# Optimization experiments

Measured on AMD Instinct MI355X. Metric: run time of the kernel, lower is better.

Reference implementation:

```python
import jax, jax.numpy as jnp
import numpy as np
import math

H, D, DFF = 12, 768, 3072
DH = D // H  # 64
B, T = 4, 2048
EPS = 1e-5


def setup_inputs() -> dict:
    key = jax.random.key(0)
    ks = jax.random.split(key, 12)
    randw = lambda k, *d: jax.random.normal(k, d, jnp.float32) / math.sqrt(d[-1])
    return {
        "X": jax.random.normal(ks[0], (B, T, D), jnp.float32),
        "w_q": randw(ks[1], H, DH, D),
        "w_k": randw(ks[2], H, DH, D),
        "w_v": randw(ks[3], H, DH, D),
        "w_o": randw(ks[4], DH * H, D),
        "W1": jax.random.normal(ks[5], (DFF, D), jnp.float32) * 0.02,
        "b1": jnp.zeros((DFF,), jnp.float32),
        "W2": jax.random.normal(ks[6], (D, DFF), jnp.float32) * 0.02,
        "b2": jnp.zeros((D,), jnp.float32),
        "g1": jnp.ones((D,), jnp.float32),
        "be1": jnp.zeros((D,), jnp.float32),
        "g2": jnp.ones((D,), jnp.float32),
        "be2": jnp.zeros((D,), jnp.float32),
    }


def layernorm(x, g, b):
    mu = jnp.mean(x, axis=-1, keepdims=True)
    var = jnp.var(x, axis=-1, keepdims=True)
    return (x - mu) * jax.lax.rsqrt(var + EPS) * g + b


def attention(x, w_q, w_k, w_v, w_o):
    # x: [n,t,c]
    q = jnp.einsum('ntc,hdc->nhtd', x, w_q)
    k = jnp.einsum('ntc,hdc->nhtd', x, w_k)
    v = jnp.einsum('ntc,hdc->nhtd', x, w_v)
    a = jnp.einsum('nhtd,nhsd->nhts', q, k) / math.sqrt(q.shape[3])
    t, s = a.shape[2], a.shape[3]
    forbidden = jnp.arange(t)[:, None] < jnp.arange(s)[None, :]
    a = jnp.where(forbidden, -jnp.inf, a)
    a = jax.nn.softmax(a, axis=3)
    y = jnp.einsum('nhts,nhsd->nthd', a, v).reshape(x.shape[0], t, -1)
    return y @ w_o


def reference(X, w_q, w_k, w_v, w_o, W1, b1, W2, b2, g1, be1, g2, be2):
    X = X + attention(layernorm(X, g1, be1), w_q, w_k, w_v, w_o)
    h = jax.nn.relu(layernorm(X, g2, be2) @ W1.T + b1)
    return X + h @ W2.T + b2
```

## Files before the change

### kernel.cpp

```cpp
#include <hip/hip_runtime.h>
#include <stdint.h>

#define B_   4
#define T_   2048
#define D_   768
#define H_   12
#define DH_  64
#define DFF_ 3072
#define NTOK_ (B_*T_)
#define QKVN_ (3*D_)

typedef unsigned short u16;
typedef __bf16 bf16x8 __attribute__((ext_vector_type(8)));
typedef float  f32x4  __attribute__((ext_vector_type(4)));

__device__ __forceinline__ u16 f2bf(float f) {
  union { float f; unsigned u; } v; v.f = f;
  return (u16)((v.u + 0x7fffu + ((v.u >> 16) & 1u)) >> 16);
}

__device__ __forceinline__ u16 f2bf_ru(float f) {
  union { float f; unsigned u; } v; v.f = f;
  return (u16)((v.u + 0x8000u) >> 16);
}

__device__ __forceinline__ float fast_exp2(float x) {
#if __has_builtin(__builtin_amdgcn_exp2f)
  return __builtin_amdgcn_exp2f(x);
#else
  return exp2f(x);
#endif
}

__device__ __forceinline__ float fast_rcp(float x) {
#if __has_builtin(__builtin_amdgcn_rcpf)
  return __builtin_amdgcn_rcpf(x);
#else
  return 1.0f / x;
#endif
}

__device__ __forceinline__ void gload_lds16(const void* g, void* l) {
  __builtin_amdgcn_global_load_lds(
      (__attribute__((address_space(1))) unsigned int*)(void*)g,
      (__attribute__((address_space(3))) unsigned int*)l, 16, 0, 0);
}

template<bool BIAS, bool RELU, bool RES, bool BF16OUT, bool QSCALE, int BN,
         bool VTRANS>
__global__ __launch_bounds__(256) void gemm_bt(
    const u16* __restrict__ A, const u16* __restrict__ Bw,
    const float* __restrict__ bias, const float* __restrict__ res,
    void* __restrict__ outp, u16* __restrict__ vtp, int M, int N, int K)
{
  constexpr int NI = BN / 32;
  __shared__ u16 lA[2 * 128 * 32];
  __shared__ u16 lB[2 * BN * 32];
  const int tid  = threadIdx.x;
  const int lane = tid & 63;
  const int wave = tid >> 6;
  const int quad = lane >> 4;
  const int l15  = lane & 15;
  const int mBase = blockIdx.x * 128;
  const int nBase = blockIdx.y * BN;
  const int wm = (wave >> 1) * 64;
  const int wn = (wave & 1) * (BN / 2);

  const f32x4 fz = {0.f, 0.f, 0.f, 0.f};
  f32x4 acc[4][NI];
#pragma unroll
  for (int i = 0; i < 4; i++)
#pragma unroll
    for (int j = 0; j < NI; j++) acc[i][j] = fz;

  const int c0 = tid, c1 = tid + 256;
  const u16* gA0 = A  + (size_t)(mBase + (c0 >> 2)) * K + (c0 & 3) * 8;
  const u16* gA1 = A  + (size_t)(mBase + (c1 >> 2)) * K + (c1 & 3) * 8;
  const u16* gB0 = Bw + (size_t)(nBase + (c0 >> 2)) * K + (c0 & 3) * 8;
  const u16* gB1 = (BN == 128)
      ? Bw + (size_t)(nBase + (c1 >> 2)) * K + (c1 & 3) * 8 : nullptr;
  u16* lA0 = lA + c0 * 8; u16* lA1 = lA + c1 * 8;
  u16* lB0 = lB + c0 * 8;
  u16* lB1 = (BN == 128) ? lB + c1 * 8 : nullptr;

  for (int kt = 0; kt < K; kt += 64) {
    gload_lds16(gA0 + kt,      lA0);
    gload_lds16(gA1 + kt,      lA1);
    gload_lds16(gA0 + kt + 32, lA0 + 128 * 32);
    gload_lds16(gA1 + kt + 32, lA1 + 128 * 32);
    gload_lds16(gB0 + kt,      lB0);
    gload_lds16(gB0 + kt + 32, lB0 + BN * 32);
    if (BN == 128) {
      gload_lds16(gB1 + kt,      lB1);
      gload_lds16(gB1 + kt + 32, lB1 + BN * 32);
    }
    __syncthreads();
#pragma unroll
    for (int hf = 0; hf < 2; hf++) {
      const u16* lAh = lA + hf * (128 * 32);
      const u16* lBh = lB + hf * (BN * 32);
      bf16x8 af[4], bfr[NI];
#pragma unroll
      for (int mi = 0; mi < 4; mi++)
        af[mi] = *(const bf16x8*)(lAh + (wm + mi * 16 + l15) * 32 + quad * 8);
#pragma unroll
      for (int ni = 0; ni < NI; ni++)
        bfr[ni] = *(const bf16x8*)(lBh + (wn + ni * 16 + l15) * 32 + quad * 8);
#pragma unroll
      for (int mi = 0; mi < 4; mi++)
#pragma unroll
        for (int ni = 0; ni < NI; ni++)
          acc[mi][ni] = __builtin_amdgcn_mfma_f32_16x16x32_bf16(
              af[mi], bfr[ni], acc[mi][ni], 0, 0, 0);
    }
    __syncthreads();
  }

#pragma unroll
  for (int mi = 0; mi < 4; mi++) {
#pragma unroll
    for (int ni = 0; ni < NI; ni++) {
      const int col = nBase + wn + ni * 16 + l15;
      if (VTRANS && col >= 2 * D_) {
        const int n  = col - 2 * D_;
        const int hh = n >> 6, dd = n & 63;
        const int row0 = mBase + wm + mi * 16 + quad * 4;
        const int bb = row0 >> 11, tt = row0 & (T_ - 1);
        ushort4 pk;
        pk.x = f2bf(acc[mi][ni][0]); pk.y = f2bf(acc[mi][ni][1]);
        pk.z = f2bf(acc[mi][ni][2]); pk.w = f2bf(acc[mi][ni][3]);
        *(ushort4*)(vtp + ((size_t)((bb * H_ + hh) * DH_ + dd)) * T_ + tt) = pk;
        continue;
      }
      float bv = 0.f;
      if (BIAS) bv = bias[col];
#pragma unroll
      for (int r = 0; r < 4; r++) {
        const int row = mBase + wm + mi * 16 + quad * 4 + r;
        float v = acc[mi][ni][r];
        if (BIAS) v += bv;
        if (RELU) v = fmaxf(v, 0.f);
        if (RES)  v += res[(size_t)row * N + col];
        if (QSCALE && col < D_) v *= 0.180336880f;
        if (BF16OUT) ((u16*)outp)[(size_t)row * N + col] = f2bf(v);
        else        ((float*)outp)[(size_t)row * N + col] = v;
      }
    }
  }
}

__global__ __launch_bounds__(256) void attn_kernel(
    const u16* __restrict__ qkv, const u16* __restrict__ vt, u16* __restrict__ Y)
{
  __shared__ u16 lK[2][64 * 64];
  __shared__ u16 lV[2][64 * 64];
  __shared__ u16 lP[4][16 * 64];
  const int tid  = threadIdx.x;
  const int lane = tid & 63;
  const int wave = tid >> 6;
  const int quad = lane >> 4;
  const int l15  = lane & 15;
  const int qt = 31 - (int)blockIdx.x;
  const int q0 = qt * 64;
  const int h  = blockIdx.y;
  const int b  = blockIdx.z;
  const int qw = q0 + wave * 16;

  bf16x8 qf0, qf1;
  {
    const u16* qp = qkv + (size_t)(b * T_ + qw + l15) * QKVN_ + h * DH_ + quad * 8;
    qf0 = *(const bf16x8*)(qp);
    qf1 = *(const bf16x8*)(qp + 32);
  }

  const f32x4 fz = {0.f, 0.f, 0.f, 0.f};
  f32x4 o[4];
#pragma unroll
  for (int i = 0; i < 4; i++) o[i] = fz;
  float lsum[4] = {0.f, 0.f, 0.f, 0.f};

  const int c0 = tid, c1 = tid + 256;
  const int r0 = c0 >> 3, j0 = (c0 & 7) ^ (r0 & 7);
  const int r1 = c1 >> 3, j1 = (c1 & 7) ^ (r1 & 7);
  const u16* gK0 = qkv + (size_t)(b * T_ + r0) * QKVN_ + D_ + h * DH_ + j0 * 8;
  const u16* gK1 = qkv + (size_t)(b * T_ + r1) * QKVN_ + D_ + h * DH_ + j1 * 8;
  const u16* gV0 = vt + (size_t)((b * H_ + h) * DH_ + r0) * T_ + j0 * 8;
  const u16* gV1 = vt + (size_t)((b * H_ + h) * DH_ + r1) * T_ + j1 * 8;

  const int njs = qt + 1;

  gload_lds16(gK0, lK[0] + c0 * 8);
  gload_lds16(gK1, lK[0] + c1 * 8);
  gload_lds16(gV0, lV[0] + c0 * 8);
  gload_lds16(gV1, lV[0] + c1 * 8);

  for (int js = 0; js < njs; js++) {
    const int cur = js & 1;
    __syncthreads();

    if (js + 1 < njs) {
      const size_t s1 = (size_t)(js + 1) * 64;
      const int nb = cur ^ 1;
      gload_lds16(gK0 + s1 * QKVN_, lK[nb] + c0 * 8);
      gload_lds16(gK1 + s1 * QKVN_, lK[nb] + c1 * 8);
      gload_lds16(gV0 + s1,         lV[nb] + c0 * 8);
      gload_lds16(gV1 + s1,         lV[nb] + c1 * 8);
    }

    const u16* lKc = lK[cur];
    const u16* lVc = lV[cur];

    f32x4 sa[4];
#pragma unroll
    for (int ni = 0; ni < 4; ni++) {
      const int row = ni * 16 + l15;
      const int sw = row & 7;
      const bf16x8 k0 = *(const bf16x8*)(lKc + row * 64 + ((quad ^ sw) * 8));
      const bf16x8 k1 = *(const bf16x8*)(lKc + row * 64 + (((4 + quad) ^ sw) * 8));
      f32x4 t = fz;
      t = __builtin_amdgcn_mfma_f32_16x16x32_bf16(qf0, k0, t, 0, 0, 0);
      t = __builtin_amdgcn_mfma_f32_16x16x32_bf16(qf1, k1, t, 0, 0, 0);
      sa[ni] = t;
    }

    bf16x8 vf0[4], vf1[4];
#pragma unroll
    for (int dt = 0; dt < 4; dt++) {
      const int row = dt * 16 + l15;
      const int sw = row & 7;
      vf0[dt] = *(const bf16x8*)(lVc + row * 64 + ((quad ^ sw) * 8));
      vf1[dt] = *(const bf16x8*)(lVc + row * 64 + (((4 + quad) ^ sw) * 8));
    }

    if (js != qt) {
#pragma unroll
      for (int ni = 0; ni < 4; ni++)
#pragma unroll
        for (int r = 0; r < 4; r++) {
          const float p = fast_exp2(sa[ni][r]);
          sa[ni][r] = p;
          lsum[r] += p;
        }
    } else {
      const int qloc = wave * 16 + quad * 4;
#pragma unroll
      for (int ni = 0; ni < 4; ni++) {
        const int sloc = ni * 16 + l15;
#pragma unroll
        for (int r = 0; r < 4; r++) {
          const float p = (sloc > qloc + r) ? 0.f : fast_exp2(sa[ni][r]);
          sa[ni][r] = p;
          lsum[r] += p;
        }
      }
    }

    u16* lp = lP[wave];
#pragma unroll
    for (int ni = 0; ni < 4; ni++) {
      const int colc = ni * 2 + (l15 >> 3);
      const int cole = l15 & 7;
#pragma unroll
      for (int r = 0; r < 4; r++) {
        const int row = quad * 4 + r;
        lp[row * 64 + ((colc ^ (row & 7)) * 8) + cole] = f2bf_ru(sa[ni][r]);
      }
    }
    __asm__ volatile("s_waitcnt lgkmcnt(0)" ::: "memory");
    const int swp = l15 & 7;
    const bf16x8 p0 = *(const bf16x8*)(lp + l15 * 64 + ((quad ^ swp) * 8));
    const bf16x8 p1 = *(const bf16x8*)(lp + l15 * 64 + (((4 + quad) ^ swp) * 8));
#pragma unroll
    for (int dt = 0; dt < 4; dt++) {
      o[dt] = __builtin_amdgcn_mfma_f32_16x16x32_bf16(p0, vf0[dt], o[dt], 0, 0, 0);
      o[dt] = __builtin_amdgcn_mfma_f32_16x16x32_bf16(p1, vf1[dt], o[dt], 0, 0, 0);
    }
  }

#pragma unroll
  for (int off = 1; off < 16; off <<= 1)
#pragma unroll
    for (int r = 0; r < 4; r++) lsum[r] += __shfl_xor(lsum[r], off);
  float rl[4];
#pragma unroll
  for (int r = 0; r < 4; r++) rl[r] = fast_rcp(lsum[r]);

#pragma unroll
  for (int dt = 0; dt < 4; dt++)
#pragma unroll
    for (int r = 0; r < 4; r++) {
      const int q = qw + quad * 4 + r;
      const int col = h * DH_ + dt * 16 + l15;
      Y[(size_t)(b * T_ + q) * D_ + col] = f2bf(o[dt][r] * rl[r]);
    }
}

__device__ __forceinline__ void ln_row(
    const float* __restrict__ X, const float* __restrict__ g,
    const float* __restrict__ be, u16* __restrict__ out, int row)
{
  const float* x = X + (size_t)row * D_;
  const int t = threadIdx.x;
  const float v0 = x[t], v1 = x[t + 256], v2 = x[t + 512];
  float s = v0 + v1 + v2;
  float sq = v0 * v0 + v1 * v1 + v2 * v2;
#pragma unroll
  for (int off = 1; off < 64; off <<= 1) {
    s  += __shfl_xor(s, off);
    sq += __shfl_xor(sq, off);
  }
  __shared__ float ws_[4], wq_[4];
  const int wv = t >> 6, lane = t & 63;
  if (lane == 0) { ws_[wv] = s; wq_[wv] = sq; }
  __syncthreads();
  s  = ws_[0] + ws_[1] + ws_[2] + ws_[3];
  sq = wq_[0] + wq_[1] + wq_[2] + wq_[3];
  const float mean = s * (1.f / 768.f);
  const float var  = sq * (1.f / 768.f) - mean * mean;
  const float rstd = rsqrtf(var + 1e-5f);
  u16* o = out + (size_t)row * D_;
  int c = t;
  o[c] = f2bf((v0 - mean) * rstd * g[c] + be[c]); c += 256;
  o[c] = f2bf((v1 - mean) * rstd * g[c] + be[c]); c += 256;
  o[c] = f2bf((v2 - mean) * rstd * g[c] + be[c]);
}

__global__ __launch_bounds__(256) void ln_kernel(
    const float* __restrict__ X, const float* __restrict__ g,
    const float* __restrict__ be, u16* __restrict__ out)
{
  ln_row(X, g, be, out, blockIdx.x);
}

__global__ __launch_bounds__(256) void prep_kernel(
    const float* __restrict__ X, const float* __restrict__ g1,
    const float* __restrict__ be1, u16* __restrict__ xln,
    const float* __restrict__ w_q, const float* __restrict__ w_k,
    const float* __restrict__ w_v, const float* __restrict__ W1,
    const float* __restrict__ W2, const float* __restrict__ w_o,
    u16* __restrict__ wqkv, u16* __restrict__ W1b,
    u16* __restrict__ W2b, u16* __restrict__ woT)
{
  if (blockIdx.x < NTOK_) {
    ln_row(X, g1, be1, xln, blockIdx.x);
    return;
  }
  const int id = blockIdx.x - NTOK_;
  if (id < 144) {
    __shared__ float tile[64][65];
    const int bx = id % 12, by = id / 12;
    const int rr0 = by * 64, cc0 = bx * 64;
    for (int idx = threadIdx.x; idx < 4096; idx += 256) {
      const int i = idx >> 6, j = idx & 63;
      tile[i][j] = w_o[(size_t)(rr0 + i) * D_ + cc0 + j];
    }
    __syncthreads();
    for (int idx = threadIdx.x; idx < 4096; idx += 256) {
      const int i = idx >> 6, j = idx & 63;
      woT[(size_t)(cc0 + i) * D_ + rr0 + j] = f2bf(tile[j][i]);
    }
  } else {
    const int WQN = H_ * DH_ * D_;
    const int i = (id - 144) * 256 + threadIdx.x;
    if (i < 3 * WQN) {
      const float* src = (i < WQN) ? w_q : (i < 2 * WQN ? w_k : w_v);
      const int off = (i < WQN) ? i : (i < 2 * WQN ? i - WQN : i - 2 * WQN);
      wqkv[i] = f2bf(src[off]);
    } else if (i < 3 * WQN + DFF_ * D_) {
      const int off = i - 3 * WQN;
      W1b[off] = f2bf(W1[off]);
    } else {
      const int off = i - 3 * WQN - DFF_ * D_;
      W2b[off] = f2bf(W2[off]);
    }
  }
}

extern "C" void kernel_launch(void* const* d_in, const int* in_sizes, int n_in,
                              void* d_out, int out_size, void* d_ws, size_t ws_size,
                              hipStream_t stream) {
  const float* X   = (const float*)d_in[0];
  const float* w_q = (const float*)d_in[1];
  const float* w_k = (const float*)d_in[2];
  const float* w_v = (const float*)d_in[3];
  const float* w_o = (const float*)d_in[4];
  const float* W1  = (const float*)d_in[5];
  const float* b1  = (const float*)d_in[6];
  const float* W2  = (const float*)d_in[7];
  const float* b2  = (const float*)d_in[8];
  const float* g1  = (const float*)d_in[9];
  const float* be1 = (const float*)d_in[10];
  const float* g2  = (const float*)d_in[11];
  const float* be2 = (const float*)d_in[12];
  float* out = (float*)d_out;

  char* ws = (char*)d_ws;
  u16*   qkv  = (u16*)(ws + 0);
  u16*   vt   = (u16*)(ws + 37748736);
  u16*   hbuf = (u16*)(ws + 0);
  u16*   xln  = (u16*)(ws + 50331648);
  u16*   Ybuf = (u16*)(ws + 62914560);
  float* X1   = (float*)(ws + 75497472);
  u16*   wqkv = (u16*)(ws + 100663296);
  u16*   woT  = (u16*)(ws + 104202240);
  u16*   W1b  = (u16*)(ws + 105381888);
  u16*   W2b  = (u16*)(ws + 110100480);

  prep_kernel<<<NTOK_ + 25488, 256, 0, stream>>>(
      X, g1, be1, xln, w_q, w_k, w_v, W1, W2, w_o, wqkv, W1b, W2b, woT);

  gemm_bt<false, false, false, true, true, 128, true>
      <<<dim3(64, 18), 256, 0, stream>>>(
      xln, wqkv, nullptr, nullptr, qkv, vt, NTOK_, QKVN_, D_);

  attn_kernel<<<dim3(32, 12, 4), 256, 0, stream>>>(qkv, vt, Ybuf);

  gemm_bt<false, false, true, false, false, 64, false>
      <<<dim3(64, 12), 256, 0, stream>>>(
      Ybuf, woT, nullptr, X, X1, nullptr, NTOK_, D_, D_);

  ln_kernel<<<NTOK_, 256, 0, stream>>>(X1, g2, be2, xln);

  gemm_bt<true, true, false, true, false, 128, false>
      <<<dim3(64, 24), 256, 0, stream>>>(
      xln, W1b, b1, nullptr, hbuf, nullptr, NTOK_, DFF_, D_);

  gemm_bt<true, false, true, false, false, 64, false>
      <<<dim3(64, 12), 256, 0, stream>>>(
      hbuf, W2b, b2, X1, out, nullptr, NTOK_, D_, DFF_);
}
```

Measured before the change: 388.7 us.

## Widen attention tiles to 128 queries and transpose MFMA operands

The attention kernel now handles 128 query rows per block, two 16-row groups per wave, so each K/V tile loaded into LDS serves twice as many queries and the grid halves. The MFMA operand order is swapped so scores come out transposed, and P is written to LDS as packed bf16 pairs in a padded layout. Row sums then reduce with only two shuffles and the output is stored as vectorized ushort4. Waves whose queries lie wholly before a key tile skip its compute. In exchange the kernel uses more registers per wave and the causal work is less evenly spread across waves, and there are fewer blocks to fill the GPU.

```diff
diff --git a/kernel.cpp b/kernel.cpp
--- a/kernel.cpp
+++ b/kernel.cpp
@@ -11,6 +11,7 @@
 #define QKVN_ (3*D_)
 
 typedef unsigned short u16;
+typedef unsigned int u32;
 typedef __bf16 bf16x8 __attribute__((ext_vector_type(8)));
 typedef float  f32x4  __attribute__((ext_vector_type(4)));
 
@@ -19,9 +20,9 @@
   return (u16)((v.u + 0x7fffu + ((v.u >> 16) & 1u)) >> 16);
 }
 
-__device__ __forceinline__ u16 f2bf_ru(float f) {
-  union { float f; unsigned u; } v; v.f = f;
-  return (u16)((v.u + 0x8000u) >> 16);
+__device__ __forceinline__ u32 pack_bf2(float a, float b) {
+  union { float f; u32 u; } ua, ub; ua.f = a; ub.f = b;
+  return ((ua.u + 0x8000u) >> 16) | ((ub.u + 0x8000u) & 0xFFFF0000u);
 }
 
 __device__ __forceinline__ float fast_exp2(float x) {
@@ -154,30 +155,32 @@
 {
   __shared__ u16 lK[2][64 * 64];
   __shared__ u16 lV[2][64 * 64];
-  __shared__ u16 lP[4][16 * 64];
+  __shared__ u32 lP[4][2 * 16 * 36];
   const int tid  = threadIdx.x;
   const int lane = tid & 63;
   const int wave = tid >> 6;
   const int quad = lane >> 4;
   const int l15  = lane & 15;
-  const int qt = 31 - (int)blockIdx.x;
-  const int q0 = qt * 64;
+  const int qt = 15 - (int)blockIdx.x;
   const int h  = blockIdx.y;
   const int b  = blockIdx.z;
-  const int qw = q0 + wave * 16;
-
-  bf16x8 qf0, qf1;
+  const int qw0 = qt * 128 + wave * 32;
+
+  bf16x8 qA0, qA1, qB0, qB1;
   {
-    const u16* qp = qkv + (size_t)(b * T_ + qw + l15) * QKVN_ + h * DH_ + quad * 8;
-    qf0 = *(const bf16x8*)(qp);
-    qf1 = *(const bf16x8*)(qp + 32);
+    const u16* qp = qkv + (size_t)(b * T_ + qw0 + l15) * QKVN_ + h * DH_ + quad * 8;
+    qA0 = *(const bf16x8*)(qp);
+    qA1 = *(const bf16x8*)(qp + 32);
+    const u16* qp2 = qp + 16 * QKVN_;
+    qB0 = *(const bf16x8*)(qp2);
+    qB1 = *(const bf16x8*)(qp2 + 32);
   }
 
   const f32x4 fz = {0.f, 0.f, 0.f, 0.f};
-  f32x4 o[4];
-#pragma unroll
-  for (int i = 0; i < 4; i++) o[i] = fz;
-  float lsum[4] = {0.f, 0.f, 0.f, 0.f};
+  f32x4 oA[4], oB[4];
+#pragma unroll
+  for (int i = 0; i < 4; i++) { oA[i] = fz; oB[i] = fz; }
+  float lsA = 0.f, lsB = 0.f;
 
   const int c0 = tid, c1 = tid + 256;
   const int r0 = c0 >> 3, j0 = (c0 & 7) ^ (r0 & 7);
@@ -187,12 +190,17 @@
   const u16* gV0 = vt + (size_t)((b * H_ + h) * DH_ + r0) * T_ + j0 * 8;
   const u16* gV1 = vt + (size_t)((b * H_ + h) * DH_ + r1) * T_ + j1 * 8;
 
-  const int njs = qt + 1;
+  const int njs = 2 * qt + 2;
 
   gload_lds16(gK0, lK[0] + c0 * 8);
   gload_lds16(gK1, lK[0] + c1 * 8);
   gload_lds16(gV0, lV[0] + c0 * 8);
   gload_lds16(gV1, lV[0] + c1 * 8);
+
+  u32* lpA = &lP[wave][0];
+  u32* lpB = &lP[wave][576];
+  const int wbase = l15 * 36 + quad * 2;
+  const int rb0   = l15 * 36 + quad * 4;
 
   for (int js = 0; js < njs; js++) {
     const int cur = js & 1;
@@ -207,92 +215,86 @@
       gload_lds16(gV1 + s1,         lV[nb] + c1 * 8);
     }
 
+    const int s0 = js * 64;
+    if (s0 > qw0 + 31) continue;
+
     const u16* lKc = lK[cur];
     const u16* lVc = lV[cur];
 
-    f32x4 sa[4];
+    f32x4 sA[4], sB[4];
 #pragma unroll
     for (int ni = 0; ni < 4; ni++) {
       const int row = ni * 16 + l15;
       const int sw = row & 7;
       const bf16x8 k0 = *(const bf16x8*)(lKc + row * 64 + ((quad ^ sw) * 8));
       const bf16x8 k1 = *(const bf16x8*)(lKc + row * 64 + (((4 + quad) ^ sw) * 8));
-      f32x4 t = fz;
-      t = __builtin_amdgcn_mfma_f32_16x16x32_bf16(qf0, k0, t, 0, 0, 0);
-      t = __builtin_amdgcn_mfma_f32_16x16x32_bf16(qf1, k1, t, 0, 0, 0);
-      sa[ni] = t;
-    }
-
-    bf16x8 vf0[4], vf1[4];
+      f32x4 tA = fz, tB = fz;
+      tA = __builtin_amdgcn_mfma_f32_16x16x32_bf16(k0, qA0, tA, 0, 0, 0);
+      tA = __builtin_amdgcn_mfma_f32_16x16x32_bf16(k1, qA1, tA, 0, 0, 0);
+      tB = __builtin_amdgcn_mfma_f32_16x16x32_bf16(k0, qB0, tB, 0, 0, 0);
+      tB = __builtin_amdgcn_mfma_f32_16x16x32_bf16(k1, qB1, tB, 0, 0, 0);
+      sA[ni] = tA; sB[ni] = tB;
+    }
+
+    const bool nm = (s0 + 63 > qw0);
+    const int qA_idx = qw0 + l15;
+    const int qB_idx = qA_idx + 16;
+#pragma unroll
+    for (int ni = 0; ni < 4; ni++) {
+      const int sbase = s0 + ni * 16 + quad * 4;
+      float pa[4], pb[4];
+#pragma unroll
+      for (int r = 0; r < 4; r++) {
+        float va = fast_exp2(sA[ni][r]);
+        float vb = fast_exp2(sB[ni][r]);
+        if (nm) {
+          if (sbase + r > qA_idx) va = 0.f;
+          if (sbase + r > qB_idx) vb = 0.f;
+        }
+        pa[r] = va; pb[r] = vb;
+        lsA += va; lsB += vb;
+      }
+      lpA[wbase + ni * 8 + 0] = pack_bf2(pa[0], pa[1]);
+      lpA[wbase + ni * 8 + 1] = pack_bf2(pa[2], pa[3]);
+      lpB[wbase + ni * 8 + 0] = pack_bf2(pb[0], pb[1]);
+      lpB[wbase + ni * 8 + 1] = pack_bf2(pb[2], pb[3]);
+    }
+    __asm__ volatile("s_waitcnt lgkmcnt(0)" ::: "memory");
+
+    const bf16x8 pA0 = *(const bf16x8*)(lpA + rb0);
+    const bf16x8 pA1 = *(const bf16x8*)(lpA + rb0 + 16);
+    const bf16x8 pB0 = *(const bf16x8*)(lpB + rb0);
+    const bf16x8 pB1 = *(const bf16x8*)(lpB + rb0 + 16);
+
 #pragma unroll
     for (int dt = 0; dt < 4; dt++) {
       const int row = dt * 16 + l15;
       const int sw = row & 7;
-      vf0[dt] = *(const bf16x8*)(lVc + row * 64 + ((quad ^ sw) * 8));
-      vf1[dt] = *(const bf16x8*)(lVc + row * 64 + (((4 + quad) ^ sw) * 8));
-    }
-
-    if (js != qt) {
-#pragma unroll
-      for (int ni = 0; ni < 4; ni++)
-#pragma unroll
-        for (int r = 0; r < 4; r++) {
-          const float p = fast_exp2(sa[ni][r]);
-          sa[ni][r] = p;
-          lsum[r] += p;
-        }
-    } else {
-      const int qloc = wave * 16 + quad * 4;
-#pragma unroll
-      for (int ni = 0; ni < 4; ni++) {
-        const int sloc = ni * 16 + l15;
-#pragma unroll
-        for (int r = 0; r < 4; r++) {
-          const float p = (sloc > qloc + r) ? 0.f : fast_exp2(sa[ni][r]);
-          sa[ni][r] = p;
-          lsum[r] += p;
-        }
-      }
-    }
-
-    u16* lp = lP[wave];
-#pragma unroll
-    for (int ni = 0; ni < 4; ni++) {
-      const int colc = ni * 2 + (l15 >> 3);
-      const int cole = l15 & 7;
-#pragma unroll
-      for (int r = 0; r < 4; r++) {
-        const int row = quad * 4 + r;
-        lp[row * 64 + ((colc ^ (row & 7)) * 8) + cole] = f2bf_ru(sa[ni][r]);
-      }
-    }
-    __asm__ volatile("s_waitcnt lgkmcnt(0)" ::: "memory");
-    const int swp = l15 & 7;
-    const bf16x8 p0 = *(const bf16x8*)(lp + l15 * 64 + ((quad ^ swp) * 8));
-    const bf16x8 p1 = *(const bf16x8*)(lp + l15 * 64 + (((4 + quad) ^ swp) * 8));
-#pragma unroll
-    for (int dt = 0; dt < 4; dt++) {
-      o[dt] = __builtin_amdgcn_mfma_f32_16x16x32_bf16(p0, vf0[dt], o[dt], 0, 0, 0);
-      o[dt] = __builtin_amdgcn_mfma_f32_16x16x32_bf16(p1, vf1[dt], o[dt], 0, 0, 0);
-    }
-  }
-
-#pragma unroll
-  for (int off = 1; off < 16; off <<= 1)
-#pragma unroll
-    for (int r = 0; r < 4; r++) lsum[r] += __shfl_xor(lsum[r], off);
-  float rl[4];
-#pragma unroll
-  for (int r = 0; r < 4; r++) rl[r] = fast_rcp(lsum[r]);
-
-#pragma unroll
-  for (int dt = 0; dt < 4; dt++)
-#pragma unroll
-    for (int r = 0; r < 4; r++) {
-      const int q = qw + quad * 4 + r;
-      const int col = h * DH_ + dt * 16 + l15;
-      Y[(size_t)(b * T_ + q) * D_ + col] = f2bf(o[dt][r] * rl[r]);
-    }
+      const bf16x8 v0 = *(const bf16x8*)(lVc + row * 64 + ((quad ^ sw) * 8));
+      const bf16x8 v1 = *(const bf16x8*)(lVc + row * 64 + (((4 + quad) ^ sw) * 8));
+      oA[dt] = __builtin_amdgcn_mfma_f32_16x16x32_bf16(v0, pA0, oA[dt], 0, 0, 0);
+      oA[dt] = __builtin_amdgcn_mfma_f32_16x16x32_bf16(v1, pA1, oA[dt], 0, 0, 0);
+      oB[dt] = __builtin_amdgcn_mfma_f32_16x16x32_bf16(v0, pB0, oB[dt], 0, 0, 0);
+      oB[dt] = __builtin_amdgcn_mfma_f32_16x16x32_bf16(v1, pB1, oB[dt], 0, 0, 0);
+    }
+  }
+
+  lsA += __shfl_xor(lsA, 16); lsA += __shfl_xor(lsA, 32);
+  lsB += __shfl_xor(lsB, 16); lsB += __shfl_xor(lsB, 32);
+  const float rlA = fast_rcp(lsA);
+  const float rlB = fast_rcp(lsB);
+
+#pragma unroll
+  for (int dt = 0; dt < 4; dt++) {
+    const int dbase = h * DH_ + dt * 16 + quad * 4;
+    ushort4 pa, pb;
+    pa.x = f2bf(oA[dt][0] * rlA); pa.y = f2bf(oA[dt][1] * rlA);
+    pa.z = f2bf(oA[dt][2] * rlA); pa.w = f2bf(oA[dt][3] * rlA);
+    pb.x = f2bf(oB[dt][0] * rlB); pb.y = f2bf(oB[dt][1] * rlB);
+    pb.z = f2bf(oB[dt][2] * rlB); pb.w = f2bf(oB[dt][3] * rlB);
+    *(ushort4*)(Y + (size_t)(b * T_ + qw0 + l15) * D_ + dbase) = pa;
+    *(ushort4*)(Y + (size_t)(b * T_ + qw0 + 16 + l15) * D_ + dbase) = pb;
+  }
 }
 
 __device__ __forceinline__ void ln_row(
@@ -413,7 +415,7 @@
       <<<dim3(64, 18), 256, 0, stream>>>(
       xln, wqkv, nullptr, nullptr, qkv, vt, NTOK_, QKVN_, D_);
 
-  attn_kernel<<<dim3(32, 12, 4), 256, 0, stream>>>(qkv, vt, Ybuf);
+  attn_kernel<<<dim3(16, 12, 4), 256, 0, stream>>>(qkv, vt, Ybuf);
 
   gemm_bt<false, false, true, false, false, 64, false>
       <<<dim3(64, 12), 256, 0, stream>>>(
```

Measured after the change: 384.9 us. No clear change (-1.0%).
